# Kernel tuning notes

Hardware: AMD Instinct MI355X
Metric: run time of the kernel (lower is better)

## Reference

```python
import jax, jax.numpy as jnp
import numpy as np
from jax import lax

V, H, B, S, NSLOT, T, G, NSW = 20000, 400, 16, 256, 30, 10, 3, 40


def setup_inputs() -> dict:
    key = jax.random.key(0)
    ks = jax.random.split(key, 24)
    p = lambda k, shape: jax.random.normal(k, shape, dtype=jnp.float32) * 0.1
    return {
        'story': jax.random.randint(ks[0], (B, S), 0, V),
        'enc_lens': jax.random.randint(ks[1], (B,), S // 2, S + 1),
        'target_batches': jax.random.randint(ks[2], (B, NSLOT, T), 0, V),
        'domain_idx': jax.random.randint(ks[3], (NSLOT,), 0, NSW),
        'slot_idx': jax.random.randint(ks[4], (NSLOT,), 0, NSW),
        'emb': p(ks[5], (V, H)),
        'enc_Wih_f': p(ks[6], (3 * H, H)), 'enc_Whh_f': p(ks[7], (3 * H, H)),
        'enc_bih_f': p(ks[8], (3 * H,)), 'enc_bhh_f': p(ks[9], (3 * H,)),
        'enc_Wih_b': p(ks[10], (3 * H, H)), 'enc_Whh_b': p(ks[11], (3 * H, H)),
        'enc_bih_b': p(ks[12], (3 * H,)), 'enc_bhh_b': p(ks[13], (3 * H,)),
        'dec_Wih': p(ks[14], (3 * H, H)), 'dec_Whh': p(ks[15], (3 * H, H)),
        'dec_bih': p(ks[16], (3 * H,)), 'dec_bhh': p(ks[17], (3 * H,)),
        'Wr': p(ks[18], (1, 3 * H)), 'br': p(ks[19], (1,)),
        'Wg': p(ks[20], (G, H)), 'bg': p(ks[21], (G,)),
        'slot_table': p(ks[22], (NSW, H)),
    }


def _gru_scan(x, m, h0, Wih, Whh, bih, bhh):
    # x: [S,B,H], m: [S,B] validity mask (packed-sequence semantics)
    def step(h, xm):
        xt, mt = xm
        gi = xt @ Wih.T + bih
        gh = h @ Whh.T + bhh
        ir, iz, inn = jnp.split(gi, 3, -1)
        hr, hz, hn = jnp.split(gh, 3, -1)
        r = jax.nn.sigmoid(ir + hr)
        z = jax.nn.sigmoid(iz + hz)
        n = jnp.tanh(inn + r * hn)
        hnew = (1.0 - z) * n + z * h
        h = jnp.where(mt[:, None], hnew, h)
        y = jnp.where(mt[:, None], hnew, 0.0)
        return h, y
    hT, ys = lax.scan(step, h0, (x, m))
    return ys, hT


def reference(story, enc_lens, target_batches, domain_idx, slot_idx, emb,
              enc_Wih_f, enc_Whh_f, enc_bih_f, enc_bhh_f,
              enc_Wih_b, enc_Whh_b, enc_bih_b, enc_bhh_b,
              dec_Wih, dec_Whh, dec_bih, dec_bhh,
              Wr, br, Wg, bg, slot_table):
    Bc, Sc = story.shape
    nslot = domain_idx.shape[0]
    Tc = target_batches.shape[2]
    NB = nslot * Bc

    # ----- EncoderRNN: bidirectional GRU over story (seq-major) -----
    x = emb[story.T]                                   # [S,B,H]
    mask = jnp.arange(Sc)[:, None] < enc_lens[None, :]  # [S,B]
    h0 = jnp.zeros((Bc, H), jnp.float32)
    ys_f, h_f = _gru_scan(x, mask, h0, enc_Wih_f, enc_Whh_f, enc_bih_f, enc_bhh_f)
    ys_b, h_b = _gru_scan(x[::-1], mask[::-1], h0, enc_Wih_b, enc_Whh_b, enc_bih_b, enc_bhh_b)
    ys_b = ys_b[::-1]
    encoded_outputs = (ys_f + ys_b).transpose(1, 0, 2)  # [B,S,H]
    enc_hidden = h_f + h_b                              # [B,H]

    # ----- Generator (parallel decode, teacher forcing) -----
    combined = slot_table[domain_idx] + slot_table[slot_idx]           # [nslot,H]
    slot_emb_arr = jnp.repeat(combined[:, None, :], Bc, axis=1).reshape(NB, H)
    hidden0 = jnp.tile(enc_hidden, (nslot, 1))                         # [NB,H]
    enc_out = jnp.tile(encoded_outputs, (nslot, 1, 1))                 # [NB,S,H]
    lens_rep = jnp.tile(enc_lens, nslot)
    story_rep = jnp.tile(story, (nslot, 1))                            # [NB,S]
    attn_mask = jnp.arange(Sc)[None, :] < lens_rep[:, None]            # [NB,S]
    rows = jnp.arange(NB)[:, None]

    # teacher-forced decoder inputs: step0 = slot emb, then gold tokens
    tgt_flat = target_batches.transpose(1, 0, 2).reshape(NB, Tc)       # [NB,T]
    dec_in = jnp.concatenate([slot_emb_arr[None], emb[tgt_flat[:, :Tc - 1].T]], axis=0)  # [T,NB,H]

    def dec_step(h, x_in):
        gi = x_in @ dec_Wih.T + dec_bih
        gh = h @ dec_Whh.T + dec_bhh
        ir, iz, inn = jnp.split(gi, 3, -1)
        hr, hz, hn = jnp.split(gh, 3, -1)
        r = jax.nn.sigmoid(ir + hr)
        z = jax.nn.sigmoid(iz + hz)
        n = jnp.tanh(inn + r * hn)
        h = (1.0 - z) * n + z * h                      # dec_state == new hidden
        scores = jnp.einsum('nh,nsh->ns', h, enc_out)
        scores = jnp.where(attn_mask, scores, -jnp.inf)
        prob = jax.nn.softmax(scores, axis=1)          # [NB,S]
        context = jnp.einsum('ns,nsh->nh', prob, enc_out)
        p_vocab = jax.nn.softmax(h @ emb.T, axis=1)    # [NB,V]
        p_gen_vec = jnp.concatenate([h, context, x_in], axis=-1)
        sw = jax.nn.sigmoid(p_gen_vec @ Wr.T + br)     # [NB,1]
        p_ctx = jnp.zeros_like(p_vocab).at[rows, story_rep].add(prob)
        final_p = (1.0 - sw) * p_ctx + sw * p_vocab
        return h, (final_p, context)

    _, (finals, contexts) = lax.scan(dec_step, hidden0, dec_in)
    all_point_outputs = finals.reshape(Tc, nslot, Bc, V).transpose(1, 2, 0, 3)  # [nslot,B,T,V]
    all_gate_outputs = (contexts[0] @ Wg.T + bg).reshape(nslot, Bc, G)
    return all_point_outputs, all_gate_outputs
```

## Files before the change

### kernel.cpp

```cpp
#include <hip/hip_runtime.h>
#include <hip/hip_bf16.h>

typedef unsigned short u16;
typedef __attribute__((ext_vector_type(8))) short bf16x8;
typedef __attribute__((ext_vector_type(4))) float f32x4;
typedef __attribute__((ext_vector_type(4))) unsigned u32x4;

static constexpr int V = 20000, H = 400, B = 16, S = 256, NSLOT = 30, T = 10, G = 3;
static constexpr int H3 = 3 * H;
static constexpr int NB = NSLOT * B;
static constexpr int MM = T * NB;
static constexpr int ENBLK = 20;
static constexpr int ESL   = 20;
static constexpr int EROWS = 64;
static constexpr int EKP   = 416;
static constexpr int HP2 = 424;
static constexpr int SCP = 260;
static constexpr int PP  = 264;
static constexpr int CXP = 404;
static constexpr int FUSED_LDS = 32*HP2*2 + 32*SCP*4 + 32*PP*2 + 32*CXP*4;

__device__ __forceinline__ float bf2f(u16 v) {
    union { unsigned u; float f; } x; x.u = ((unsigned)v) << 16; return x.f;
}
__device__ __forceinline__ u16 f2bf(float f) {
    union { float f; unsigned u; } x; x.f = f;
    unsigned r = x.u + 0x7fffu + ((x.u >> 16) & 1u);
    return (u16)(r >> 16);
}
__device__ __forceinline__ float sigm(float v) { return 1.f / (1.f + __expf(-v)); }

__global__ __launch_bounds__(256) void gemm_bt(
    const u16* __restrict__ A, const u16* __restrict__ Bt,
    const float* __restrict__ bias, float* __restrict__ C,
    int M, int N, int K, int lda, int ldb, long long ldc,
    long long sA, long long sB, long long sC,
    int mode, float* __restrict__ rowsum)
{
    __shared__ u16 As[64][40];
    __shared__ u16 Bs[64][40];
    const int bz = blockIdx.z;
    A  += (long long)bz * sA;
    Bt += (long long)bz * sB;
    C  += (long long)bz * sC;
    const int m0 = blockIdx.x * 64, n0 = blockIdx.y * 64;
    const int tid = threadIdx.x, wave = tid >> 6, lane = tid & 63;
    const int wm = (wave >> 1) * 32, wn = (wave & 1) * 32;
    const int srow = tid >> 2, scol = (tid & 3) * 8;
    const int fr = lane & 15, kq = lane >> 4;
    f32x4 acc[2][2];
#pragma unroll
    for (int i = 0; i < 2; ++i)
#pragma unroll
        for (int j = 0; j < 2; ++j) acc[i][j] = (f32x4){0.f, 0.f, 0.f, 0.f};

    for (int k0 = 0; k0 < K; k0 += 32) {
        {
            int gr = m0 + srow, gc = k0 + scol;
            bf16x8 v;
            if (gr < M && gc + 8 <= K) {
                v = *(const bf16x8*)(A + (long long)gr * lda + gc);
            } else {
                short tmp[8];
#pragma unroll
                for (int j = 0; j < 8; ++j)
                    tmp[j] = (gr < M && gc + j < K) ? (short)A[(long long)gr * lda + gc + j] : (short)0;
                v = *(bf16x8*)tmp;
            }
            *(bf16x8*)&As[srow][scol] = v;
        }
        {
            int gr = n0 + srow, gc = k0 + scol;
            bf16x8 v;
            if (gr < N && gc + 8 <= K) {
                v = *(const bf16x8*)(Bt + (long long)gr * ldb + gc);
            } else {
                short tmp[8];
#pragma unroll
                for (int j = 0; j < 8; ++j)
                    tmp[j] = (gr < N && gc + j < K) ? (short)Bt[(long long)gr * ldb + gc + j] : (short)0;
                v = *(bf16x8*)tmp;
            }
            *(bf16x8*)&Bs[srow][scol] = v;
        }
        __syncthreads();
        bf16x8 af[2], bfr[2];
#pragma unroll
        for (int i = 0; i < 2; ++i) af[i]  = *(const bf16x8*)&As[wm + i * 16 + fr][kq * 8];
#pragma unroll
        for (int j = 0; j < 2; ++j) bfr[j] = *(const bf16x8*)&Bs[wn + j * 16 + fr][kq * 8];
#pragma unroll
        for (int i = 0; i < 2; ++i)
#pragma unroll
            for (int j = 0; j < 2; ++j)
                acc[i][j] = __builtin_amdgcn_mfma_f32_16x16x32_bf16(af[i], bfr[j], acc[i][j], 0, 0, 0);
        __syncthreads();
    }

#pragma unroll
    for (int i = 0; i < 2; ++i)
#pragma unroll
        for (int j = 0; j < 2; ++j) {
            int col = n0 + wn + j * 16 + fr;
            float bv = (bias != nullptr && col < N) ? bias[col] : 0.f;
#pragma unroll
            for (int r = 0; r < 4; ++r) {
                int row = m0 + wm + i * 16 + kq * 4 + r;
                bool ok = (row < M) && (col < N);
                float v = acc[i][j][r] + bv;
                if (mode >= 1) { v = ok ? __expf(v) : 0.f; acc[i][j][r] = v; }
                if (ok) C[(long long)row * ldc + col] = v;
            }
        }
    if (mode >= 1) {
#pragma unroll
        for (int i = 0; i < 2; ++i)
#pragma unroll
            for (int r = 0; r < 4; ++r) {
                float s = acc[i][0][r] + acc[i][1][r];
                s += __shfl_xor(s, 1); s += __shfl_xor(s, 2);
                s += __shfl_xor(s, 4); s += __shfl_xor(s, 8);
                if (fr == 0) {
                    int row = m0 + wm + i * 16 + kq * 4 + r;
                    if (row < M) atomicAdd(&rowsum[row], s);
                }
            }
    }
}

__global__ __launch_bounds__(256) void vocab_gemm_kernel(
    const u16* __restrict__ A, const u16* __restrict__ Bt,
    float* __restrict__ C, float* __restrict__ rowsum)
{
    __shared__ u16 As[128][40];
    __shared__ u16 Bs[128][40];
    const int m0 = blockIdx.x * 128, n0 = blockIdx.y * 128;
    const int tid = threadIdx.x, wave = tid >> 6, lane = tid & 63;
    const int wm = (wave >> 1) * 64, wn = (wave & 1) * 64;
    const int srow = tid >> 1, scol = (tid & 1) * 16;
    const int fr = lane & 15, kq = lane >> 4;
    f32x4 acc[4][4];
#pragma unroll
    for (int i = 0; i < 4; ++i)
#pragma unroll
        for (int j = 0; j < 4; ++j) acc[i][j] = (f32x4){0.f, 0.f, 0.f, 0.f};

    for (int k0 = 0; k0 < H; k0 += 32) {
        {
            int gr = m0 + srow, gc = k0 + scol;
            bf16x8 v0 = (bf16x8){0,0,0,0,0,0,0,0}, v1 = v0;
            if (gr < MM) {
                const u16* src = A + (long long)gr * H + gc;
                if (gc + 8 <= H)  v0 = *(const bf16x8*)src;
                if (gc + 16 <= H) v1 = *(const bf16x8*)(src + 8);
            }
            *(bf16x8*)&As[srow][scol] = v0;
            *(bf16x8*)&As[srow][scol + 8] = v1;
        }
        {
            int gr = n0 + srow, gc = k0 + scol;
            bf16x8 v0 = (bf16x8){0,0,0,0,0,0,0,0}, v1 = v0;
            if (gr < V) {
                const u16* src = Bt + (long long)gr * H + gc;
                if (gc + 8 <= H)  v0 = *(const bf16x8*)src;
                if (gc + 16 <= H) v1 = *(const bf16x8*)(src + 8);
            }
            *(bf16x8*)&Bs[srow][scol] = v0;
            *(bf16x8*)&Bs[srow][scol + 8] = v1;
        }
        __syncthreads();
        bf16x8 af[4], bfr[4];
#pragma unroll
        for (int i = 0; i < 4; ++i) af[i]  = *(const bf16x8*)&As[wm + i * 16 + fr][kq * 8];
#pragma unroll
        for (int j = 0; j < 4; ++j) bfr[j] = *(const bf16x8*)&Bs[wn + j * 16 + fr][kq * 8];
#pragma unroll
        for (int i = 0; i < 4; ++i)
#pragma unroll
            for (int j = 0; j < 4; ++j)
                acc[i][j] = __builtin_amdgcn_mfma_f32_16x16x32_bf16(af[i], bfr[j], acc[i][j], 0, 0, 0);
        __syncthreads();
    }

#pragma unroll
    for (int i = 0; i < 4; ++i)
#pragma unroll
        for (int j = 0; j < 4; ++j)
#pragma unroll
            for (int r = 0; r < 4; ++r) {
                int row = m0 + wm + i * 16 + kq * 4 + r;
                int col = n0 + wn + j * 16 + fr;
                bool ok = (row < MM) && (col < V);
                float v = ok ? __expf(acc[i][j][r]) : 0.f;
                acc[i][j][r] = v;
                if (ok) {
                    int n = row % NB, t = row / NB;
                    C[((long long)n * T + t) * V + col] = v;
                }
            }
#pragma unroll
    for (int i = 0; i < 4; ++i)
#pragma unroll
        for (int r = 0; r < 4; ++r) {
            float s = acc[i][0][r] + acc[i][1][r] + acc[i][2][r] + acc[i][3][r];
            s += __shfl_xor(s, 1); s += __shfl_xor(s, 2);
            s += __shfl_xor(s, 4); s += __shfl_xor(s, 8);
            if (fr == 0) {
                int row = m0 + wm + i * 16 + kq * 4 + r;
                if (row < MM) atomicAdd(&rowsum[row], s);
            }
        }
}

__global__ void cvt_bf16_kernel(const float* __restrict__ src, u16* __restrict__ dst, int n) {
    for (int i = blockIdx.x * blockDim.x + threadIdx.x; i < n; i += gridDim.x * blockDim.x)
        dst[i] = f2bf(src[i]);
}

__global__ void cvt4_kernel(const float* __restrict__ a, const float* __restrict__ b,
                            const float* __restrict__ c, const float* __restrict__ d,
                            u16* __restrict__ da, u16* __restrict__ db,
                            u16* __restrict__ dc, u16* __restrict__ dd, int n) {
    for (int i = blockIdx.x * blockDim.x + threadIdx.x; i < n; i += gridDim.x * blockDim.x) {
        da[i] = f2bf(a[i]); db[i] = f2bf(b[i]); dc[i] = f2bf(c[i]); dd[i] = f2bf(d[i]);
    }
}

__global__ void prep_wenc_kernel(const float* __restrict__ whhf, const float* __restrict__ whhb,
                                 u16* __restrict__ dst) {
    int idx = blockIdx.x * 256 + threadIdx.x;
    const int total = 2 * ENBLK * EROWS * EKP;
    if (idx >= total) return;
    int k = idx % EKP; int r = idx / EKP;
    int rloc = r % EROWS; r /= EROWS;
    int j = r % ENBLK; int dir = r / ENBLK;
    u16 v = 0;
    if (k < H && rloc < 3 * ESL) {
        int g = rloc / ESL, c = rloc % ESL;
        const float* W = dir ? whhb : whhf;
        v = f2bf(W[(long long)(g * H + j * ESL + c) * H + k]);
    }
    dst[idx] = v;
}

__global__ void embed_story_kernel(const int* __restrict__ story, const u16* __restrict__ embb,
                                   u16* __restrict__ xb) {
    int row = blockIdx.x;
    int s = row >> 4, b = row & 15;
    int tok = story[b * S + s];
    const u16* e = embb + (long long)tok * H;
    u16* d = xb + (long long)row * H;
    for (int k = threadIdx.x; k < H; k += blockDim.x) d[k] = e[k];
}

__global__ void build_decin_kernel(const int* __restrict__ tgt, const int* __restrict__ dom,
                                   const int* __restrict__ sidx, const float* __restrict__ slt,
                                   const u16* __restrict__ embb, u16* __restrict__ decin) {
    int n = blockIdx.x, t = blockIdx.y;
    int b = n & 15, slot = n >> 4;
    u16* d = decin + ((long long)t * NB + n) * H;
    if (t == 0) {
        const float* s1 = slt + (long long)dom[slot] * H;
        const float* s2 = slt + (long long)sidx[slot] * H;
        for (int k = threadIdx.x; k < H; k += blockDim.x) d[k] = f2bf(s1[k] + s2[k]);
    } else {
        int tok = tgt[(b * NSLOT + slot) * T + (t - 1)];
        const u16* e = embb + (long long)tok * H;
        for (int k = threadIdx.x; k < H; k += blockDim.x) d[k] = e[k];
    }
}

__global__ __launch_bounds__(256) void enc_rnn2_kernel(
    const u16* __restrict__ wencp,
    const float* __restrict__ bhhf, const float* __restrict__ bhhb,
    const float* __restrict__ gif, const float* __restrict__ gib,
    const int* __restrict__ lens,
    unsigned* __restrict__ hbuf, int* __restrict__ flags,
    float* __restrict__ ysf, float* __restrict__ ysb,
    float* __restrict__ hfo, float* __restrict__ hbo)
{
    const int bid = blockIdx.x;
    const int dir = bid / ENBLK, j = bid % ENBLK;
    const float* bhh = dir ? bhhb : bhhf;
    const float* gi  = dir ? gib  : gif;
    float* ys = dir ? ysb : ysf;
    float* ho = dir ? hbo : hfo;

    __shared__ u16 wlds[EROWS * EKP];
    __shared__ float ghs[EROWS * 17];

    const int tid = threadIdx.x, wave = tid >> 6, lane = tid & 63;
    const int fr = lane & 15, kq = lane >> 4;

    const u16* wsrc = wencp + (long long)(dir * ENBLK + j) * EROWS * EKP;
    for (int i = tid * 8; i < EROWS * EKP; i += 256 * 8)
        *(bf16x8*)&wlds[i] = *(const bf16x8*)&wsrc[i];
    for (int i = tid; i < EROWS * 17; i += 256) ghs[i] = 0.f;

    const int p0 = tid, p1 = 256 + tid;
    const bool has1 = (tid < 64);
    const int b0 = p0 / ESL, kl0 = p0 % ESL;
    const int b1 = has1 ? p1 / ESL : 0, kl1 = has1 ? p1 % ESL : 0;
    const int k0 = j * ESL;
    const int len0 = lens[b0];
    const int len1 = has1 ? lens[b1] : 0;
    const float bhr0 = bhh[k0 + kl0], bhz0 = bhh[H + k0 + kl0], bhn0 = bhh[2 * H + k0 + kl0];
    const float bhr1 = has1 ? bhh[k0 + kl1] : 0.f;
    const float bhz1 = has1 ? bhh[H + k0 + kl1] : 0.f;
    const float bhn1 = has1 ? bhh[2 * H + k0 + kl1] : 0.f;
    float h0r = 0.f, h1r = 0.f;

    unsigned* hb_d = hbuf + (long long)dir * S * B * EKP;
    int* flg_d = flags + dir * S * ENBLK;
    const u16* arow = &wlds[(wave * 16 + fr) * EKP + kq * 8];
    __syncthreads();

    for (int t = 0; t < S; ++t) {
        const int s = dir ? (S - 1 - t) : t;
        const float* gbase = gi + (long long)s * B * H3;
        float gr0 = gbase[b0 * H3 + k0 + kl0];
        float gz0 = gbase[b0 * H3 + H + k0 + kl0];
        float gn0 = gbase[b0 * H3 + 2 * H + k0 + kl0];
        float gr1 = 0.f, gz1 = 0.f, gn1 = 0.f;
        if (has1) {
            gr1 = gbase[b1 * H3 + k0 + kl1];
            gz1 = gbase[b1 * H3 + H + k0 + kl1];
            gn1 = gbase[b1 * H3 + 2 * H + k0 + kl1];
        }

        f32x4 acc = (f32x4){0.f, 0.f, 0.f, 0.f};
        if (t > 0) {
            const int* fl = flg_d + (t - 1) * ENBLK;
            for (;;) {
                int v = 1;
                if (lane < ENBLK)
                    v = __hip_atomic_load(&fl[lane], __ATOMIC_RELAXED,
                                          __HIP_MEMORY_SCOPE_AGENT);
                if (__all(v != 0)) break;
                __builtin_amdgcn_s_sleep(2);
            }
            asm volatile("" ::: "memory");
            const unsigned* hrow = hb_d + ((long long)(t - 1) * B + fr) * EKP + kq * 8;
            f32x4 acch = (f32x4){0.f, 0.f, 0.f, 0.f};
            f32x4 accl = (f32x4){0.f, 0.f, 0.f, 0.f};
#pragma unroll
            for (int kk = 0; kk < 13; ++kk) {
                u32x4 a = *(const u32x4*)(hrow + kk * 32);
                u32x4 b = *(const u32x4*)(hrow + kk * 32 + 4);
                union { unsigned u[4]; bf16x8 v; } hi, lo;
                hi.u[0] = __builtin_amdgcn_perm(a[1], a[0], 0x05040100u);
                hi.u[1] = __builtin_amdgcn_perm(a[3], a[2], 0x05040100u);
                hi.u[2] = __builtin_amdgcn_perm(b[1], b[0], 0x05040100u);
                hi.u[3] = __builtin_amdgcn_perm(b[3], b[2], 0x05040100u);
                lo.u[0] = __builtin_amdgcn_perm(a[1], a[0], 0x07060302u);
                lo.u[1] = __builtin_amdgcn_perm(a[3], a[2], 0x07060302u);
                lo.u[2] = __builtin_amdgcn_perm(b[1], b[0], 0x07060302u);
                lo.u[3] = __builtin_amdgcn_perm(b[3], b[2], 0x07060302u);
                bf16x8 av = *(const bf16x8*)(arow + kk * 32);
                acch = __builtin_amdgcn_mfma_f32_16x16x32_bf16(av, hi.v, acch, 0, 0, 0);
                accl = __builtin_amdgcn_mfma_f32_16x16x32_bf16(av, lo.v, accl, 0, 0, 0);
            }
            acc = acch + accl;
        }
#pragma unroll
        for (int r = 0; r < 4; ++r) ghs[(wave * 16 + kq * 4 + r) * 17 + fr] = acc[r];
        __syncthreads();

        unsigned* hpub = hb_d + (long long)t * B * EKP;
        {
            float ghr = ghs[kl0 * 17 + b0];
            float ghz = ghs[(ESL + kl0) * 17 + b0];
            float ghn = ghs[(2 * ESL + kl0) * 17 + b0];
            float rg = sigm(gr0 + ghr + bhr0);
            float zg = sigm(gz0 + ghz + bhz0);
            float ng = tanhf(gn0 + rg * (ghn + bhn0));
            float hn = (1.f - zg) * ng + zg * h0r;
            bool msk = s < len0;
            float y = msk ? hn : 0.f;
            if (msk) h0r = hn;
            ys[((long long)(b0 * S + s)) * H + k0 + kl0] = y;
            u16 hi = f2bf(h0r);
            unsigned packed = (unsigned)hi | ((unsigned)f2bf(h0r - bf2f(hi)) << 16);
            __hip_atomic_store(&hpub[b0 * EKP + k0 + kl0], packed, __ATOMIC_RELAXED,
                               __HIP_MEMORY_SCOPE_AGENT);
        }
        if (has1) {
            float ghr = ghs[kl1 * 17 + b1];
            float ghz = ghs[(ESL + kl1) * 17 + b1];
            float ghn = ghs[(2 * ESL + kl1) * 17 + b1];
            float rg = sigm(gr1 + ghr + bhr1);
            float zg = sigm(gz1 + ghz + bhz1);
            float ng = tanhf(gn1 + rg * (ghn + bhn1));
            float hn = (1.f - zg) * ng + zg * h1r;
            bool msk = s < len1;
            float y = msk ? hn : 0.f;
            if (msk) h1r = hn;
            ys[((long long)(b1 * S + s)) * H + k0 + kl1] = y;
            u16 hi = f2bf(h1r);
            unsigned packed = (unsigned)hi | ((unsigned)f2bf(h1r - bf2f(hi)) << 16);
            __hip_atomic_store(&hpub[b1 * EKP + k0 + kl1], packed, __ATOMIC_RELAXED,
                               __HIP_MEMORY_SCOPE_AGENT);
        }
        __syncthreads();
        if (tid == 0)
            __hip_atomic_store(&flg_d[t * ENBLK + j], 1, __ATOMIC_RELAXED,
                               __HIP_MEMORY_SCOPE_AGENT);
    }
    ho[b0 * H + k0 + kl0] = h0r;
    if (has1) ho[b1 * H + k0 + kl1] = h1r;
}

__global__ void packE_kernel(const float* __restrict__ ysf, const float* __restrict__ ysb,
                             u16* __restrict__ E, u16* __restrict__ ET) {
    __shared__ u16 tile[32][400];
    const int b = blockIdx.x, s0 = blockIdx.y * 32;
    for (int si = 0; si < 32; ++si) {
        const long long base = ((long long)b * S + s0 + si) * H;
        for (int k = threadIdx.x; k < H; k += blockDim.x) {
            u16 v = f2bf(ysf[base + k] + ysb[base + k]);
            E[base + k] = v;
            tile[si][k] = v;
        }
    }
    __syncthreads();
    for (int idx = threadIdx.x; idx < 32 * H; idx += blockDim.x) {
        int k = idx >> 5, si = idx & 31;
        ET[((long long)b * H + k) * S + s0 + si] = tile[si][k];
    }
}

__global__ void h0_kernel(const float* __restrict__ hf, const float* __restrict__ hb,
                          float* __restrict__ hf32, u16* __restrict__ hnk) {
    int n = blockIdx.x, b = n & 15;
    for (int k = threadIdx.x; k < H; k += blockDim.x) {
        float v = hf[b * H + k] + hb[b * H + k];
        hf32[(long long)n * H + k] = v;
        hnk[(long long)n * H + k] = f2bf(v);
    }
}

__global__ __launch_bounds__(512) void fused_step_kernel(
    const float* __restrict__ dgi, const float* __restrict__ dgh,
    float* __restrict__ hf32, u16* __restrict__ hall,
    const u16* __restrict__ decinb,
    const u16* __restrict__ Eb, const u16* __restrict__ ETb,
    const int* __restrict__ lens,
    const float* __restrict__ Wr, const float* __restrict__ br,
    const float* __restrict__ Wg, const float* __restrict__ bg,
    float* __restrict__ probfT, float* __restrict__ swvT,
    float* __restrict__ gout, int t)
{
    extern __shared__ char smem[];
    u16*   hls = (u16*)smem;
    float* scs = (float*)(smem + 32 * HP2 * 2);
    u16*   pls = (u16*)(smem + 32 * HP2 * 2 + 32 * SCP * 4);
    float* cxs = (float*)(smem + 32 * HP2 * 2 + 32 * SCP * 4 + 32 * PP * 2);

    const int b = blockIdx.x;
    const int tid = threadIdx.x, wave = tid >> 6, lane = tid & 63;
    const int fr = lane & 15, kq = lane >> 4;
    const int len = lens[b];

    for (int i = tid; i < 32 * (HP2 - H); i += 512) {
        int r = i / (HP2 - H), c = H + i % (HP2 - H);
        hls[r * HP2 + c] = 0;
    }
    for (int i = tid; i < 2 * HP2; i += 512) hls[30 * HP2 + i] = 0;
    for (int i = tid; i < 2 * PP; i += 512) pls[30 * PP + i] = 0;

    for (int i = tid; i < 30 * H; i += 512) {
        int slot = i / H, k = i % H;
        int n = slot * 16 + b;
        const float* gi = dgi + ((long long)t * NB + n) * H3;
        const float* gh = dgh + (long long)n * H3;
        float r  = sigm(gi[k] + gh[k]);
        float z  = sigm(gi[H + k] + gh[H + k]);
        float nn = tanhf(gi[2 * H + k] + r * gh[2 * H + k]);
        float h  = hf32[(long long)n * H + k];
        float hn = (1.f - z) * nn + z * h;
        hf32[(long long)n * H + k] = hn;
        u16 hb = f2bf(hn);
        hall[((long long)t * NB + n) * H + k] = hb;
        hls[slot * HP2 + k] = hb;
    }
    __syncthreads();

    {
        const int nt0 = wave * 2;
        f32x4 acc[2][2];
#pragma unroll
        for (int i = 0; i < 2; ++i)
#pragma unroll
            for (int jj = 0; jj < 2; ++jj) acc[i][jj] = (f32x4){0.f, 0.f, 0.f, 0.f};
        const u16* br0 = Eb + ((long long)b * S + nt0 * 16 + fr) * H + kq * 8;
        const u16* br1 = Eb + ((long long)b * S + (nt0 + 1) * 16 + fr) * H + kq * 8;
        const u16* ar0 = hls + fr * HP2 + kq * 8;
        const u16* ar1 = hls + (16 + fr) * HP2 + kq * 8;
#pragma unroll
        for (int kk = 0; kk < 13; ++kk) {
            bf16x8 av0 = *(const bf16x8*)(ar0 + kk * 32);
            bf16x8 av1 = *(const bf16x8*)(ar1 + kk * 32);
            bf16x8 bv0, bv1;
            if (kk == 12 && kq >= 2) {
                bv0 = (bf16x8){0,0,0,0,0,0,0,0}; bv1 = bv0;
            } else {
                bv0 = *(const bf16x8*)(br0 + kk * 32);
                bv1 = *(const bf16x8*)(br1 + kk * 32);
            }
            acc[0][0] = __builtin_amdgcn_mfma_f32_16x16x32_bf16(av0, bv0, acc[0][0], 0, 0, 0);
            acc[1][0] = __builtin_amdgcn_mfma_f32_16x16x32_bf16(av1, bv0, acc[1][0], 0, 0, 0);
            acc[0][1] = __builtin_amdgcn_mfma_f32_16x16x32_bf16(av0, bv1, acc[0][1], 0, 0, 0);
            acc[1][1] = __builtin_amdgcn_mfma_f32_16x16x32_bf16(av1, bv1, acc[1][1], 0, 0, 0);
        }
#pragma unroll
        for (int i = 0; i < 2; ++i)
#pragma unroll
            for (int jj = 0; jj < 2; ++jj)
#pragma unroll
                for (int r = 0; r < 4; ++r)
                    scs[(i * 16 + kq * 4 + r) * SCP + (nt0 + jj) * 16 + fr] = acc[i][jj][r];
    }
    __syncthreads();

    for (int i = 0; i < 4; ++i) {
        int row = wave * 4 + i;
        if (row >= 30) break;
        int n = row * 16 + b;
        float v[4];
        float mx = -3.0e38f;
#pragma unroll
        for (int q = 0; q < 4; ++q) {
            int s = lane + 64 * q;
            float x = (s < len) ? scs[row * SCP + s] : -3.0e38f;
            v[q] = x; mx = fmaxf(mx, x);
        }
        mx = fmaxf(mx, __shfl_xor(mx, 1));  mx = fmaxf(mx, __shfl_xor(mx, 2));
        mx = fmaxf(mx, __shfl_xor(mx, 4));  mx = fmaxf(mx, __shfl_xor(mx, 8));
        mx = fmaxf(mx, __shfl_xor(mx, 16)); mx = fmaxf(mx, __shfl_xor(mx, 32));
        float sum = 0.f;
#pragma unroll
        for (int q = 0; q < 4; ++q) {
            int s = lane + 64 * q;
            float e = (s < len) ? __expf(v[q] - mx) : 0.f;
            v[q] = e; sum += e;
        }
        sum += __shfl_xor(sum, 1);  sum += __shfl_xor(sum, 2);
        sum += __shfl_xor(sum, 4);  sum += __shfl_xor(sum, 8);
        sum += __shfl_xor(sum, 16); sum += __shfl_xor(sum, 32);
        float inv = 1.f / sum;
#pragma unroll
        for (int q = 0; q < 4; ++q) {
            int s = lane + 64 * q;
            float pr = v[q] * inv;
            pls[row * PP + s] = f2bf(pr);
            probfT[((long long)(t * NB + n)) * S + s] = pr;
        }
    }
    __syncthreads();

    for (int nt = wave; nt < 25; nt += 8) {
        f32x4 acc0 = (f32x4){0.f,0.f,0.f,0.f}, acc1 = (f32x4){0.f,0.f,0.f,0.f};
        const u16* brow = ETb + ((long long)b * H + nt * 16 + fr) * S + kq * 8;
        const u16* ar0 = pls + fr * PP + kq * 8;
        const u16* ar1 = pls + (16 + fr) * PP + kq * 8;
#pragma unroll
        for (int kk = 0; kk < 8; ++kk) {
            bf16x8 bv  = *(const bf16x8*)(brow + kk * 32);
            bf16x8 av0 = *(const bf16x8*)(ar0 + kk * 32);
            bf16x8 av1 = *(const bf16x8*)(ar1 + kk * 32);
            acc0 = __builtin_amdgcn_mfma_f32_16x16x32_bf16(av0, bv, acc0, 0, 0, 0);
            acc1 = __builtin_amdgcn_mfma_f32_16x16x32_bf16(av1, bv, acc1, 0, 0, 0);
        }
#pragma unroll
        for (int r = 0; r < 4; ++r) {
            cxs[(kq * 4 + r) * CXP + nt * 16 + fr] = acc0[r];
            cxs[(16 + kq * 4 + r) * CXP + nt * 16 + fr] = acc1[r];
        }
    }
    __syncthreads();

    for (int i = 0; i < 4; ++i) {
        int slot = wave + 8 * i;
        if (slot >= 30) break;
        int n = slot * 16 + b;
        const u16* xrow = decinb + ((long long)t * NB + n) * H;
        float p = 0.f;
        for (int k = lane; k < H; k += 64)
            p += bf2f(hls[slot * HP2 + k]) * Wr[k]
               + cxs[slot * CXP + k] * Wr[H + k]
               + bf2f(xrow[k]) * Wr[2 * H + k];
        p += __shfl_xor(p, 1);  p += __shfl_xor(p, 2);
        p += __shfl_xor(p, 4);  p += __shfl_xor(p, 8);
        p += __shfl_xor(p, 16); p += __shfl_xor(p, 32);
        if (lane == 0) swvT[t * NB + n] = sigm(p + br[0]);
        if (t == 0) {
            for (int g = 0; g < G; ++g) {
                float q = 0.f;
                for (int k = lane; k < H; k += 64)
                    q += cxs[slot * CXP + k] * Wg[g * H + k];
                q += __shfl_xor(q, 1);  q += __shfl_xor(q, 2);
                q += __shfl_xor(q, 4);  q += __shfl_xor(q, 8);
                q += __shfl_xor(q, 16); q += __shfl_xor(q, 32);
                if (lane == 0) gout[(long long)n * G + g] = q + bg[g];
            }
        }
    }
}

__global__ void scale_all_kernel(float* __restrict__ out, const float* __restrict__ swvT,
                                 const float* __restrict__ rowsumT) {
    const int n = blockIdx.x;
    const int col = blockIdx.y * 256 + threadIdx.x;
    if (col >= V) return;
#pragma unroll
    for (int t = 0; t < T; ++t) {
        float f = swvT[t * NB + n] / rowsumT[t * NB + n];
        out[((long long)n * T + t) * V + col] *= f;
    }
}

__global__ void scatter_all_kernel(float* __restrict__ out, const int* __restrict__ story,
                                   const int* __restrict__ lens, const float* __restrict__ swvT,
                                   const float* __restrict__ probfT) {
    const int n = blockIdx.x, t = blockIdx.y, b = n & 15, s = threadIdx.x;
    if (s < lens[b]) {
        int tok = story[b * S + s];
        atomicAdd(out + ((long long)n * T + t) * V + tok,
                  (1.f - swvT[t * NB + n]) * probfT[((long long)(t * NB + n)) * S + s]);
    }
}

extern "C" void kernel_launch(void* const* d_in, const int* in_sizes, int n_in,
                              void* d_out, int out_size, void* d_ws, size_t ws_size,
                              hipStream_t stream) {
    const int*   story = (const int*)d_in[0];
    const int*   lens  = (const int*)d_in[1];
    const int*   tgt   = (const int*)d_in[2];
    const int*   dom   = (const int*)d_in[3];
    const int*   sidx  = (const int*)d_in[4];
    const float* emb   = (const float*)d_in[5];
    const float* wihf  = (const float*)d_in[6];
    const float* whhf  = (const float*)d_in[7];
    const float* bihf  = (const float*)d_in[8];
    const float* bhhf  = (const float*)d_in[9];
    const float* wihb  = (const float*)d_in[10];
    const float* whhb  = (const float*)d_in[11];
    const float* bihb  = (const float*)d_in[12];
    const float* bhhb  = (const float*)d_in[13];
    const float* dwih  = (const float*)d_in[14];
    const float* dwhh  = (const float*)d_in[15];
    const float* dbih  = (const float*)d_in[16];
    const float* dbhh  = (const float*)d_in[17];
    const float* Wr    = (const float*)d_in[18];
    const float* br    = (const float*)d_in[19];
    const float* Wg    = (const float*)d_in[20];
    const float* bg    = (const float*)d_in[21];
    const float* slt   = (const float*)d_in[22];
    float* out = (float*)d_out;

    char* wsb = (char*)d_ws;
    size_t off = 0;
    auto alloc = [&](size_t bytes) -> char* {
        char* p = wsb + off;
        off += (bytes + 255) & ~(size_t)255;
        return p;
    };
    u16*   embb   = (u16*)alloc((size_t)V * H * 2);
    u16*   wihfb  = (u16*)alloc((size_t)H3 * H * 2);
    u16*   wihbb  = (u16*)alloc((size_t)H3 * H * 2);
    u16*   dwihb  = (u16*)alloc((size_t)H3 * H * 2);
    u16*   dwhhb  = (u16*)alloc((size_t)H3 * H * 2);
    u16*   wencp  = (u16*)alloc((size_t)2 * ENBLK * EROWS * EKP * 2);
    unsigned* hbuf = (unsigned*)alloc((size_t)2 * S * B * EKP * 4);
    int*   flags  = (int*)alloc((size_t)2 * S * ENBLK * 4);
    u16*   xb     = (u16*)alloc((size_t)S * B * H * 2);
    u16*   decinb = (u16*)alloc((size_t)T * NB * H * 2);
    float* gif    = (float*)alloc((size_t)S * B * H3 * 4);
    float* gib    = (float*)alloc((size_t)S * B * H3 * 4);
    float* dgi    = (float*)alloc((size_t)T * NB * H3 * 4);
    float* ysf    = (float*)alloc((size_t)B * S * H * 4);
    float* ysb    = (float*)alloc((size_t)B * S * H * 4);
    float* hfv    = (float*)alloc((size_t)B * H * 4);
    float* hbv    = (float*)alloc((size_t)B * H * 4);
    u16*   Eb     = (u16*)alloc((size_t)B * S * H * 2);
    u16*   ETb    = (u16*)alloc((size_t)B * H * S * 2);
    float* hf32   = (float*)alloc((size_t)NB * H * 4);
    u16*   hnk    = (u16*)alloc((size_t)NB * H * 2);
    u16*   hall   = (u16*)alloc((size_t)T * NB * H * 2);
    float* dgh    = (float*)alloc((size_t)NB * H3 * 4);
    float* probfT = (float*)alloc((size_t)T * NB * S * 4);
    float* swvT   = (float*)alloc((size_t)T * NB * 4);
    float* rowsumT = (float*)alloc((size_t)T * NB * 4);
    (void)ws_size; (void)in_sizes; (void)n_in; (void)out_size;

    auto launch_gemm = [&](const u16* A, const u16* Bt, const float* bias, float* C,
                           int M, int N, int K, int lda, int ldb, long long ldc,
                           long long sA, long long sB, long long sC, int nb,
                           int mode, float* rs) {
        dim3 g((M + 63) / 64, (N + 63) / 64, nb);
        gemm_bt<<<g, 256, 0, stream>>>(A, Bt, bias, C, M, N, K, lda, ldb, ldc,
                                       sA, sB, sC, mode, rs);
    };

    hipFuncSetAttribute((const void*)fused_step_kernel,
                        hipFuncAttributeMaxDynamicSharedMemorySize, FUSED_LDS);

    cvt_bf16_kernel<<<2048, 256, 0, stream>>>(emb, embb, V * H);
    cvt4_kernel<<<1024, 256, 0, stream>>>(wihf, wihb, dwih, dwhh,
                                          wihfb, wihbb, dwihb, dwhhb, H3 * H);
    {
        const int total = 2 * ENBLK * EROWS * EKP;
        prep_wenc_kernel<<<(total + 255) / 256, 256, 0, stream>>>(whhf, whhb, wencp);
    }
    embed_story_kernel<<<S * B, 256, 0, stream>>>(story, embb, xb);
    { dim3 g(NB, T); build_decin_kernel<<<g, 256, 0, stream>>>(tgt, dom, sidx, slt, embb, decinb); }

    launch_gemm(xb, wihfb, bihf, gif, S * B, H3, H, H, H, H3, 0, 0, 0, 1, 0, nullptr);
    launch_gemm(xb, wihbb, bihb, gib, S * B, H3, H, H, H, H3, 0, 0, 0, 1, 0, nullptr);
    launch_gemm(decinb, dwihb, dbih, dgi, T * NB, H3, H, H, H, H3, 0, 0, 0, 1, 0, nullptr);

    hipMemsetAsync(flags, 0, (size_t)2 * S * ENBLK * 4, stream);
    hipMemsetAsync(hbuf, 0, (size_t)2 * S * B * EKP * 4, stream);
    hipMemsetAsync(rowsumT, 0, (size_t)T * NB * 4, stream);
    enc_rnn2_kernel<<<2 * ENBLK, 256, 0, stream>>>(wencp, bhhf, bhhb, gif, gib, lens,
                                                   hbuf, flags, ysf, ysb, hfv, hbv);
    { dim3 g(B, S / 32); packE_kernel<<<g, 256, 0, stream>>>(ysf, ysb, Eb, ETb); }
    h0_kernel<<<NB, 256, 0, stream>>>(hfv, hbv, hf32, hnk);

    for (int t = 0; t < T; ++t) {
        const u16* hprev = (t == 0) ? hnk : hall + (size_t)(t - 1) * NB * H;
        launch_gemm(hprev, dwhhb, dbhh, dgh, NB, H3, H, H, H, H3, 0, 0, 0, 1, 0, nullptr);
        fused_step_kernel<<<16, 512, FUSED_LDS, stream>>>(
            dgi, dgh, hf32, hall, decinb, Eb, ETb, lens, Wr, br, Wg, bg,
            probfT, swvT, out + (size_t)NB * T * V, t);
    }

    {
        dim3 g((MM + 127) / 128, (V + 127) / 128);
        vocab_gemm_kernel<<<g, 256, 0, stream>>>(hall, embb, out, rowsumT);
    }
    { dim3 g(NB, (V + 255) / 256); scale_all_kernel<<<g, 256, 0, stream>>>(out, swvT, rowsumT); }
    { dim3 g(NB, T); scatter_all_kernel<<<g, 256, 0, stream>>>(out, story, lens, swvT, probfT); }
}
```

Measured before the change: 2.424 ms.

## Merge prep kernels and overlap decoder input GEMM with encoder RNN

Merges the weight conversion and packing kernels into one prep kernel, and the story embedding and decoder-input kernels into one. The two encoder input GEMMs become a single launch indexed by grid z. The decoder input-projection GEMM tiles are appended as extra blocks to the latency-bound encoder recurrence kernel so they run on otherwise idle CUs. This removes several launches and hides the dgi GEMM behind the sequential encoder, but it relies on the encoder's flag-based inter-block spin sync not deadlocking when GEMM blocks take CU slots.

```diff
diff --git a/kernel.cpp b/kernel.cpp
--- a/kernel.cpp
+++ b/kernel.cpp
@@ -14,11 +14,18 @@
 static constexpr int ESL   = 20;
 static constexpr int EROWS = 64;
 static constexpr int EKP   = 416;
+static constexpr int ENC_BLOCKS = 2 * ENBLK;
+static constexpr int DGI_TM = (MM + 63) / 64;
+static constexpr int DGI_TN = (H3 + 63) / 64;
+static constexpr int DGI_TILES = DGI_TM * DGI_TN;
 static constexpr int HP2 = 424;
 static constexpr int SCP = 260;
 static constexpr int PP  = 264;
 static constexpr int CXP = 404;
 static constexpr int FUSED_LDS = 32*HP2*2 + 32*SCP*4 + 32*PP*2 + 32*CXP*4;
+static constexpr int NE = V * H;
+static constexpr int NW = H3 * H;
+static constexpr int NP = 2 * ENBLK * EROWS * EKP;
 
 __device__ __forceinline__ float bf2f(u16 v) {
     union { unsigned u; float f; } x; x.u = ((unsigned)v) << 16; return x.f;
@@ -33,16 +40,10 @@
 __global__ __launch_bounds__(256) void gemm_bt(
     const u16* __restrict__ A, const u16* __restrict__ Bt,
     const float* __restrict__ bias, float* __restrict__ C,
-    int M, int N, int K, int lda, int ldb, long long ldc,
-    long long sA, long long sB, long long sC,
-    int mode, float* __restrict__ rowsum)
+    int M, int N, int K, int lda, int ldb, long long ldc)
 {
     __shared__ u16 As[64][40];
     __shared__ u16 Bs[64][40];
-    const int bz = blockIdx.z;
-    A  += (long long)bz * sA;
-    Bt += (long long)bz * sB;
-    C  += (long long)bz * sC;
     const int m0 = blockIdx.x * 64, n0 = blockIdx.y * 64;
     const int tid = threadIdx.x, wave = tid >> 6, lane = tid & 63;
     const int wm = (wave >> 1) * 32, wn = (wave & 1) * 32;
@@ -106,26 +107,75 @@
 #pragma unroll
             for (int r = 0; r < 4; ++r) {
                 int row = m0 + wm + i * 16 + kq * 4 + r;
-                bool ok = (row < M) && (col < N);
-                float v = acc[i][j][r] + bv;
-                if (mode >= 1) { v = ok ? __expf(v) : 0.f; acc[i][j][r] = v; }
-                if (ok) C[(long long)row * ldc + col] = v;
-            }
-        }
-    if (mode >= 1) {
+                if (row < M && col < N) C[(long long)row * ldc + col] = acc[i][j][r] + bv;
+            }
+        }
+}
+
+__global__ __launch_bounds__(256) void gemm_xw2_kernel(
+    const u16* __restrict__ A,
+    const u16* __restrict__ W0, const u16* __restrict__ W1,
+    const float* __restrict__ b0, const float* __restrict__ b1,
+    float* __restrict__ C0, float* __restrict__ C1)
+{
+    const int z = blockIdx.z;
+    const u16* Bt = z ? W1 : W0;
+    const float* bias = z ? b1 : b0;
+    float* C = z ? C1 : C0;
+    const int M = S * B, N = H3, K = H;
+
+    __shared__ u16 As[64][40];
+    __shared__ u16 Bs[64][40];
+    const int m0 = blockIdx.x * 64, n0 = blockIdx.y * 64;
+    const int tid = threadIdx.x, wave = tid >> 6, lane = tid & 63;
+    const int wm = (wave >> 1) * 32, wn = (wave & 1) * 32;
+    const int srow = tid >> 2, scol = (tid & 3) * 8;
+    const int fr = lane & 15, kq = lane >> 4;
+    f32x4 acc[2][2];
+#pragma unroll
+    for (int i = 0; i < 2; ++i)
+#pragma unroll
+        for (int j = 0; j < 2; ++j) acc[i][j] = (f32x4){0.f, 0.f, 0.f, 0.f};
+
+    for (int k0 = 0; k0 < K; k0 += 32) {
+        {
+            int gr = m0 + srow, gc = k0 + scol;
+            bf16x8 v = (bf16x8){0,0,0,0,0,0,0,0};
+            if (gr < M && gc + 8 <= K) v = *(const bf16x8*)(A + (long long)gr * K + gc);
+            *(bf16x8*)&As[srow][scol] = v;
+        }
+        {
+            int gr = n0 + srow, gc = k0 + scol;
+            bf16x8 v = (bf16x8){0,0,0,0,0,0,0,0};
+            if (gr < N && gc + 8 <= K) v = *(const bf16x8*)(Bt + (long long)gr * K + gc);
+            *(bf16x8*)&Bs[srow][scol] = v;
+        }
+        __syncthreads();
+        bf16x8 af[2], bfr[2];
+#pragma unroll
+        for (int i = 0; i < 2; ++i) af[i]  = *(const bf16x8*)&As[wm + i * 16 + fr][kq * 8];
+#pragma unroll
+        for (int j = 0; j < 2; ++j) bfr[j] = *(const bf16x8*)&Bs[wn + j * 16 + fr][kq * 8];
 #pragma unroll
         for (int i = 0; i < 2; ++i)
 #pragma unroll
+            for (int j = 0; j < 2; ++j)
+                acc[i][j] = __builtin_amdgcn_mfma_f32_16x16x32_bf16(af[i], bfr[j], acc[i][j], 0, 0, 0);
+        __syncthreads();
+    }
+
+#pragma unroll
+    for (int i = 0; i < 2; ++i)
+#pragma unroll
+        for (int j = 0; j < 2; ++j) {
+            int col = n0 + wn + j * 16 + fr;
+            float bv = (col < N) ? bias[col] : 0.f;
+#pragma unroll
             for (int r = 0; r < 4; ++r) {
-                float s = acc[i][0][r] + acc[i][1][r];
-                s += __shfl_xor(s, 1); s += __shfl_xor(s, 2);
-                s += __shfl_xor(s, 4); s += __shfl_xor(s, 8);
-                if (fr == 0) {
-                    int row = m0 + wm + i * 16 + kq * 4 + r;
-                    if (row < M) atomicAdd(&rowsum[row], s);
-                }
-            }
-    }
+                int row = m0 + wm + i * 16 + kq * 4 + r;
+                if (row < M && col < N) C[(long long)row * H3 + col] = acc[i][j][r] + bv;
+            }
+        }
 }
 
 __global__ __launch_bounds__(256) void vocab_gemm_kernel(
@@ -212,85 +262,149 @@
         }
 }
 
-__global__ void cvt_bf16_kernel(const float* __restrict__ src, u16* __restrict__ dst, int n) {
-    for (int i = blockIdx.x * blockDim.x + threadIdx.x; i < n; i += gridDim.x * blockDim.x)
-        dst[i] = f2bf(src[i]);
-}
-
-__global__ void cvt4_kernel(const float* __restrict__ a, const float* __restrict__ b,
-                            const float* __restrict__ c, const float* __restrict__ d,
-                            u16* __restrict__ da, u16* __restrict__ db,
-                            u16* __restrict__ dc, u16* __restrict__ dd, int n) {
-    for (int i = blockIdx.x * blockDim.x + threadIdx.x; i < n; i += gridDim.x * blockDim.x) {
-        da[i] = f2bf(a[i]); db[i] = f2bf(b[i]); dc[i] = f2bf(c[i]); dd[i] = f2bf(d[i]);
-    }
-}
-
-__global__ void prep_wenc_kernel(const float* __restrict__ whhf, const float* __restrict__ whhb,
-                                 u16* __restrict__ dst) {
-    int idx = blockIdx.x * 256 + threadIdx.x;
-    const int total = 2 * ENBLK * EROWS * EKP;
-    if (idx >= total) return;
-    int k = idx % EKP; int r = idx / EKP;
-    int rloc = r % EROWS; r /= EROWS;
-    int j = r % ENBLK; int dir = r / ENBLK;
-    u16 v = 0;
-    if (k < H && rloc < 3 * ESL) {
-        int g = rloc / ESL, c = rloc % ESL;
-        const float* W = dir ? whhb : whhf;
-        v = f2bf(W[(long long)(g * H + j * ESL + c) * H + k]);
-    }
-    dst[idx] = v;
-}
-
-__global__ void embed_story_kernel(const int* __restrict__ story, const u16* __restrict__ embb,
-                                   u16* __restrict__ xb) {
+__global__ void prep_all_kernel(
+    const float* __restrict__ emb, u16* __restrict__ embb,
+    const float* __restrict__ wihf, u16* __restrict__ wihfb,
+    const float* __restrict__ wihb, u16* __restrict__ wihbb,
+    const float* __restrict__ dwih, u16* __restrict__ dwihb,
+    const float* __restrict__ dwhh, u16* __restrict__ dwhhb,
+    const float* __restrict__ whhf, const float* __restrict__ whhb,
+    u16* __restrict__ wencp)
+{
+    const int total = NE + 4 * NW + NP;
+    for (int i = blockIdx.x * blockDim.x + threadIdx.x; i < total;
+         i += gridDim.x * blockDim.x) {
+        if (i < NE) { embb[i] = f2bf(emb[i]); continue; }
+        int i2 = i - NE;
+        if (i2 < NW) { wihfb[i2] = f2bf(wihf[i2]); continue; }
+        i2 -= NW;
+        if (i2 < NW) { wihbb[i2] = f2bf(wihb[i2]); continue; }
+        i2 -= NW;
+        if (i2 < NW) { dwihb[i2] = f2bf(dwih[i2]); continue; }
+        i2 -= NW;
+        if (i2 < NW) { dwhhb[i2] = f2bf(dwhh[i2]); continue; }
+        i2 -= NW;
+        int k = i2 % EKP; int r = i2 / EKP;
+        int rloc = r % EROWS; r /= EROWS;
+        int j = r % ENBLK; int dir = r / ENBLK;
+        u16 v = 0;
+        if (k < H && rloc < 3 * ESL) {
+            int g = rloc / ESL, c = rloc % ESL;
+            const float* W = dir ? whhb : whhf;
+            v = f2bf(W[(long long)(g * H + j * ESL + c) * H + k]);
+        }
+        wencp[i2] = v;
+    }
+}
+
+__global__ void embed_decin_kernel(
+    const int* __restrict__ story, const u16* __restrict__ embb,
+    u16* __restrict__ xb,
+    const int* __restrict__ tgt, const int* __restrict__ dom,
+    const int* __restrict__ sidx, const float* __restrict__ slt,
+    u16* __restrict__ decin)
+{
     int row = blockIdx.x;
-    int s = row >> 4, b = row & 15;
-    int tok = story[b * S + s];
-    const u16* e = embb + (long long)tok * H;
-    u16* d = xb + (long long)row * H;
-    for (int k = threadIdx.x; k < H; k += blockDim.x) d[k] = e[k];
-}
-
-__global__ void build_decin_kernel(const int* __restrict__ tgt, const int* __restrict__ dom,
-                                   const int* __restrict__ sidx, const float* __restrict__ slt,
-                                   const u16* __restrict__ embb, u16* __restrict__ decin) {
-    int n = blockIdx.x, t = blockIdx.y;
-    int b = n & 15, slot = n >> 4;
-    u16* d = decin + ((long long)t * NB + n) * H;
-    if (t == 0) {
-        const float* s1 = slt + (long long)dom[slot] * H;
-        const float* s2 = slt + (long long)sidx[slot] * H;
-        for (int k = threadIdx.x; k < H; k += blockDim.x) d[k] = f2bf(s1[k] + s2[k]);
+    if (row < S * B) {
+        int s = row >> 4, b = row & 15;
+        int tok = story[b * S + s];
+        const u16* e = embb + (long long)tok * H;
+        u16* d = xb + (long long)row * H;
+        for (int k = threadIdx.x; k < H; k += blockDim.x) d[k] = e[k];
     } else {
-        int tok = tgt[(b * NSLOT + slot) * T + (t - 1)];
-        const u16* e = embb + (long long)tok * H;
-        for (int k = threadIdx.x; k < H; k += blockDim.x) d[k] = e[k];
-    }
-}
-
-__global__ __launch_bounds__(256) void enc_rnn2_kernel(
+        int i = row - S * B;
+        int t = i / NB, n = i % NB;
+        int b = n & 15, slot = n >> 4;
+        u16* d = decin + ((long long)t * NB + n) * H;
+        if (t == 0) {
+            const float* s1 = slt + (long long)dom[slot] * H;
+            const float* s2 = slt + (long long)sidx[slot] * H;
+            for (int k = threadIdx.x; k < H; k += blockDim.x) d[k] = f2bf(s1[k] + s2[k]);
+        } else {
+            int tok = tgt[(b * NSLOT + slot) * T + (t - 1)];
+            const u16* e = embb + (long long)tok * H;
+            for (int k = threadIdx.x; k < H; k += blockDim.x) d[k] = e[k];
+        }
+    }
+}
+
+__global__ __launch_bounds__(256) void enc_dgi_kernel(
     const u16* __restrict__ wencp,
     const float* __restrict__ bhhf, const float* __restrict__ bhhb,
     const float* __restrict__ gif, const float* __restrict__ gib,
     const int* __restrict__ lens,
     unsigned* __restrict__ hbuf, int* __restrict__ flags,
     float* __restrict__ ysf, float* __restrict__ ysb,
-    float* __restrict__ hfo, float* __restrict__ hbo)
+    float* __restrict__ hfo, float* __restrict__ hbo,
+    const u16* __restrict__ decinb, const u16* __restrict__ dwhib,
+    const float* __restrict__ dbih, float* __restrict__ dgi)
 {
+    __shared__ __align__(16) char ldsu[EROWS * EKP * 2 + EROWS * 17 * 4];
+    const int tid = threadIdx.x, wave = tid >> 6, lane = tid & 63;
+    const int fr = lane & 15, kq = lane >> 4;
+
+    if (blockIdx.x >= ENC_BLOCKS) {
+        u16* As = (u16*)ldsu;
+        u16* Bs = As + 64 * 40;
+        const int tile = blockIdx.x - ENC_BLOCKS;
+        const int m0 = (tile % DGI_TM) * 64, n0 = (tile / DGI_TM) * 64;
+        const int wm = (wave >> 1) * 32, wn = (wave & 1) * 32;
+        const int srow = tid >> 2, scol = (tid & 3) * 8;
+        f32x4 acc[2][2];
+#pragma unroll
+        for (int i = 0; i < 2; ++i)
+#pragma unroll
+            for (int j = 0; j < 2; ++j) acc[i][j] = (f32x4){0.f, 0.f, 0.f, 0.f};
+
+        for (int k0 = 0; k0 < H; k0 += 32) {
+            {
+                int gr = m0 + srow, gc = k0 + scol;
+                bf16x8 v = (bf16x8){0,0,0,0,0,0,0,0};
+                if (gr < MM && gc + 8 <= H) v = *(const bf16x8*)(decinb + (long long)gr * H + gc);
+                *(bf16x8*)&As[srow * 40 + scol] = v;
+            }
+            {
+                int gr = n0 + srow, gc = k0 + scol;
+                bf16x8 v = (bf16x8){0,0,0,0,0,0,0,0};
+                if (gr < H3 && gc + 8 <= H) v = *(const bf16x8*)(dwhib + (long long)gr * H + gc);
+                *(bf16x8*)&Bs[srow * 40 + scol] = v;
+            }
+            __syncthreads();
+            bf16x8 af[2], bfr[2];
+#pragma unroll
+            for (int i = 0; i < 2; ++i) af[i]  = *(const bf16x8*)&As[(wm + i * 16 + fr) * 40 + kq * 8];
+#pragma unroll
+            for (int j = 0; j < 2; ++j) bfr[j] = *(const bf16x8*)&Bs[(wn + j * 16 + fr) * 40 + kq * 8];
+#pragma unroll
+            for (int i = 0; i < 2; ++i)
+#pragma unroll
+                for (int j = 0; j < 2; ++j)
+                    acc[i][j] = __builtin_amdgcn_mfma_f32_16x16x32_bf16(af[i], bfr[j], acc[i][j], 0, 0, 0);
+            __syncthreads();
+        }
+#pragma unroll
+        for (int i = 0; i < 2; ++i)
+#pragma unroll
+            for (int j = 0; j < 2; ++j) {
+                int col = n0 + wn + j * 16 + fr;
+                float bv = (col < H3) ? dbih[col] : 0.f;
+#pragma unroll
+                for (int r = 0; r < 4; ++r) {
+                    int row = m0 + wm + i * 16 + kq * 4 + r;
+                    if (row < MM && col < H3) dgi[(long long)row * H3 + col] = acc[i][j][r] + bv;
+                }
+            }
+        return;
+    }
+
+    u16* wlds = (u16*)ldsu;
+    float* ghs = (float*)(ldsu + EROWS * EKP * 2);
     const int bid = blockIdx.x;
     const int dir = bid / ENBLK, j = bid % ENBLK;
     const float* bhh = dir ? bhhb : bhhf;
     const float* gi  = dir ? gib  : gif;
     float* ys = dir ? ysb : ysf;
     float* ho = dir ? hbo : hfo;
-
-    __shared__ u16 wlds[EROWS * EKP];
-    __shared__ float ghs[EROWS * 17];
-
-    const int tid = threadIdx.x, wave = tid >> 6, lane = tid & 63;
-    const int fr = lane & 15, kq = lane >> 4;
 
     const u16* wsrc = wencp + (long long)(dir * ENBLK + j) * EROWS * EKP;
     for (int i = tid * 8; i < EROWS * EKP; i += 256 * 8)
@@ -693,43 +807,35 @@
     float* rowsumT = (float*)alloc((size_t)T * NB * 4);
     (void)ws_size; (void)in_sizes; (void)n_in; (void)out_size;
 
-    auto launch_gemm = [&](const u16* A, const u16* Bt, const float* bias, float* C,
-                           int M, int N, int K, int lda, int ldb, long long ldc,
-                           long long sA, long long sB, long long sC, int nb,
-                           int mode, float* rs) {
-        dim3 g((M + 63) / 64, (N + 63) / 64, nb);
-        gemm_bt<<<g, 256, 0, stream>>>(A, Bt, bias, C, M, N, K, lda, ldb, ldc,
-                                       sA, sB, sC, mode, rs);
-    };
-
     hipFuncSetAttribute((const void*)fused_step_kernel,
                         hipFuncAttributeMaxDynamicSharedMemorySize, FUSED_LDS);
-
-    cvt_bf16_kernel<<<2048, 256, 0, stream>>>(emb, embb, V * H);
-    cvt4_kernel<<<1024, 256, 0, stream>>>(wihf, wihb, dwih, dwhh,
-                                          wihfb, wihbb, dwihb, dwhhb, H3 * H);
-    {
-        const int total = 2 * ENBLK * EROWS * EKP;
-        prep_wenc_kernel<<<(total + 255) / 256, 256, 0, stream>>>(whhf, whhb, wencp);
-    }
-    embed_story_kernel<<<S * B, 256, 0, stream>>>(story, embb, xb);
-    { dim3 g(NB, T); build_decin_kernel<<<g, 256, 0, stream>>>(tgt, dom, sidx, slt, embb, decinb); }
-
-    launch_gemm(xb, wihfb, bihf, gif, S * B, H3, H, H, H, H3, 0, 0, 0, 1, 0, nullptr);
-    launch_gemm(xb, wihbb, bihb, gib, S * B, H3, H, H, H, H3, 0, 0, 0, 1, 0, nullptr);
-    launch_gemm(decinb, dwihb, dbih, dgi, T * NB, H3, H, H, H, H3, 0, 0, 0, 1, 0, nullptr);
 
     hipMemsetAsync(flags, 0, (size_t)2 * S * ENBLK * 4, stream);
     hipMemsetAsync(hbuf, 0, (size_t)2 * S * B * EKP * 4, stream);
     hipMemsetAsync(rowsumT, 0, (size_t)T * NB * 4, stream);
-    enc_rnn2_kernel<<<2 * ENBLK, 256, 0, stream>>>(wencp, bhhf, bhhb, gif, gib, lens,
-                                                   hbuf, flags, ysf, ysb, hfv, hbv);
+    prep_all_kernel<<<2048, 256, 0, stream>>>(emb, embb, wihf, wihfb, wihb, wihbb,
+                                              dwih, dwihb, dwhh, dwhhb,
+                                              whhf, whhb, wencp);
+    embed_decin_kernel<<<S * B + T * NB, 256, 0, stream>>>(
+        story, embb, xb, tgt, dom, sidx, slt, decinb);
+    {
+        dim3 g((S * B + 63) / 64, (H3 + 63) / 64, 2);
+        gemm_xw2_kernel<<<g, 256, 0, stream>>>(xb, wihfb, wihbb, bihf, bihb, gif, gib);
+    }
+
+    enc_dgi_kernel<<<ENC_BLOCKS + DGI_TILES, 256, 0, stream>>>(
+        wencp, bhhf, bhhb, gif, gib, lens, hbuf, flags, ysf, ysb, hfv, hbv,
+        decinb, dwihb, dbih, dgi);
     { dim3 g(B, S / 32); packE_kernel<<<g, 256, 0, stream>>>(ysf, ysb, Eb, ETb); }
     h0_kernel<<<NB, 256, 0, stream>>>(hfv, hbv, hf32, hnk);
 
     for (int t = 0; t < T; ++t) {
         const u16* hprev = (t == 0) ? hnk : hall + (size_t)(t - 1) * NB * H;
-        launch_gemm(hprev, dwhhb, dbhh, dgh, NB, H3, H, H, H, H3, 0, 0, 0, 1, 0, nullptr);
+        {
+            dim3 g((NB + 63) / 64, (H3 + 63) / 64);
+            gemm_bt<<<g, 256, 0, stream>>>(hprev, dwhhb, dbhh, dgh,
+                                           NB, H3, H, H, H, H3);
+        }
         fused_step_kernel<<<16, 512, FUSED_LDS, stream>>>(
             dgi, dgh, hf32, hall, decinb, Eb, ETb, lens, Wr, br, Wg, bg,
             probfT, swvT, out + (size_t)NB * T * V, t);
```

After: 2.403 ms. About the same (-0.9%).
